# Kernel tuning notes

Hardware: AMD Instinct MI355X
Metric: run time of the kernel (lower is better)

The kernel has to match this reference:

```python
import jax, jax.numpy as jnp
import numpy as np


def _log_adjacency(feats, temperature):
    """'ours' euclidean adjacency: -pairwise_dist * exp(temperature), row log_softmax."""
    B = feats.shape[0]
    f = feats.reshape(B, -1)                      # (B, D)
    diff = f[:, None, :] - f[None, :, :]          # (B, B, D) as in the torch code
    sq = jnp.sum(diff * diff, axis=-1)            # (B, B) squared distances
    # safe sqrt: zero distance on the diagonal, zero (sub)gradient like torch norm
    dist = jnp.where(sq > 0, jnp.sqrt(jnp.where(sq > 0, sq, 1.0)), 0.0)
    pre_softmax = -dist * jnp.exp(temperature)
    return jax.nn.log_softmax(pre_softmax, axis=1)


def setup_inputs() -> dict:
    key = jax.random.key(0)
    k1, k2 = jax.random.split(key)
    B, C, P, D = 128, 64, 32, 128
    image_feats = jax.random.normal(k1, (B, C, D), dtype=jnp.float32)
    lang_feats = jax.random.normal(k2, (B, P, D), dtype=jnp.float32)
    temperature = jnp.float32(np.log(0.5))  # learnable temperature param init
    return {"image_feats": image_feats, "lang_feats": lang_feats, "temperature": temperature}


def reference(image_feats, lang_feats, temperature):
    A_f = _log_adjacency(image_feats, temperature)   # (B, B) log-probs
    A_g = _log_adjacency(lang_feats, temperature)    # (B, B) log-probs (log target)
    # F.kl_div(A_f, A_g, log_target=True, reduction='none') = exp(A_g) * (A_g - A_f)
    kl = jnp.exp(A_g) * (A_g - A_f)
    return kl.sum(axis=0)                            # (B,)
```

## Files before the change

### kernel.cpp

```cpp
#include <hip/hip_runtime.h>
#include <hip/hip_bf16.h>
#include <math.h>


#define NROW 128
#define PAIRS 16384
#define D0 8192
#define D1 4096
#define CK 64
#define NC0 128
#define NC1 64
#define NCHUNK 192

typedef short v8s  __attribute__((ext_vector_type(8)));
typedef float v16f __attribute__((ext_vector_type(16)));

union Frag {
    v8s s;
    __hip_bfloat162 h[4];
};

__device__ __forceinline__ void splitPair(float a, float b, Frag& hi, Frag& lo, int idx) {
    __hip_bfloat162 h = __float22bfloat162_rn(make_float2(a, b));
    const float ra = a - __bfloat162float(h.x);
    const float rb = b - __bfloat162float(h.y);
    __hip_bfloat162 l = __float22bfloat162_rn(make_float2(ra, rb));
    hi.h[idx] = h;
    lo.h[idx] = l;
}

__device__ __forceinline__ void loadFrag(const float* __restrict__ p, Frag& hi, Frag& lo) {
    const float4 v0 = *(const float4*)(p);
    const float4 v1 = *(const float4*)(p + 4);
    splitPair(v0.x, v0.y, hi, lo, 0);
    splitPair(v0.z, v0.w, hi, lo, 1);
    splitPair(v1.x, v1.y, hi, lo, 2);
    splitPair(v1.z, v1.w, hi, lo, 3);
}

__global__ __launch_bounds__(256) void k_gram(
    const float* __restrict__ F0, const float* __restrict__ F1,
    float* __restrict__ partials, float* __restrict__ diagP,
    float* __restrict__ out)
{
    const int b = blockIdx.x;
    const int t = threadIdx.x;
    if (b == 0 && t < NROW) out[t] = 0.0f;

    const float* F; int D, k0;
    if (b < NC0) { F = F0; D = D0; k0 = b * CK; }
    else         { F = F1; D = D1; k0 = (b - NC0) * CK; }

    const int wave  = t >> 6;
    const int wy    = wave >> 1;
    const int wx    = wave & 1;
    const int lane  = t & 63;
    const int r32   = lane & 31;
    const int khalf = lane >> 5;

    const int rA0 = wy * 64 + r32;
    const int rA1 = wy * 64 + 32 + r32;
    const int rB0 = wx * 64 + r32;
    const int rB1 = wx * 64 + 32 + r32;

    v16f acc[2][2];
#pragma unroll
    for (int ti = 0; ti < 2; ++ti)
#pragma unroll
        for (int tj = 0; tj < 2; ++tj)
#pragma unroll
            for (int r = 0; r < 16; ++r) acc[ti][tj][r] = 0.0f;

#pragma unroll
    for (int g = 0; g < CK / 16; ++g) {
        const int col = k0 + g * 16 + khalf * 8;
        Frag Ah[2], Al[2], Bh[2], Bl[2];
        loadFrag(F + (size_t)rA0 * D + col, Ah[0], Al[0]);
        loadFrag(F + (size_t)rA1 * D + col, Ah[1], Al[1]);
        loadFrag(F + (size_t)rB0 * D + col, Bh[0], Bl[0]);
        loadFrag(F + (size_t)rB1 * D + col, Bh[1], Bl[1]);
#pragma unroll
        for (int ti = 0; ti < 2; ++ti)
#pragma unroll
            for (int tj = 0; tj < 2; ++tj) {
                acc[ti][tj] = __builtin_amdgcn_mfma_f32_32x32x16_bf16(
                    Ah[ti].s, Bh[tj].s, acc[ti][tj], 0, 0, 0);
                acc[ti][tj] = __builtin_amdgcn_mfma_f32_32x32x16_bf16(
                    Ah[ti].s, Bl[tj].s, acc[ti][tj], 0, 0, 0);
                acc[ti][tj] = __builtin_amdgcn_mfma_f32_32x32x16_bf16(
                    Al[ti].s, Bh[tj].s, acc[ti][tj], 0, 0, 0);
                acc[ti][tj] = __builtin_amdgcn_mfma_f32_32x32x16_bf16(
                    Al[ti].s, Bl[tj].s, acc[ti][tj], 0, 0, 0);
            }
    }

    float* __restrict__ pout = partials + (size_t)b * PAIRS;
#pragma unroll
    for (int ti = 0; ti < 2; ++ti)
#pragma unroll
        for (int tj = 0; tj < 2; ++tj) {
            const int rowbase = wy * 64 + ti * 32;
            const int n = wx * 64 + tj * 32 + r32;
#pragma unroll
            for (int r = 0; r < 16; ++r) {
                const int m = rowbase + (r & 3) + 8 * (r >> 2) + 4 * khalf;
                const float v = acc[ti][tj][r];
                pout[m * NROW + n] = v;
                if (m == n) diagP[b * NROW + m] = v;
            }
        }
}

__device__ __forceinline__ float waveMax64(float v) {
#pragma unroll
    for (int off = 32; off > 0; off >>= 1) v = fmaxf(v, __shfl_xor(v, off, 64));
    return v;
}
__device__ __forceinline__ float waveSum64(float v) {
#pragma unroll
    for (int off = 32; off > 0; off >>= 1) v += __shfl_xor(v, off, 64);
    return v;
}

__global__ __launch_bounds__(256) void k_kl(
    const float* __restrict__ partials, const float* __restrict__ diagP,
    const float* __restrict__ temp, float* __restrict__ out)
{
    __shared__ float red[4];
    __shared__ float gii_s[2];
    __shared__ float Arow[2][NROW];

    const int i = blockIdx.x;
    const int t = threadIdx.x;
    const int s = t >> 7;
    const int j = t & 127;
    const int w = t >> 6;
    const float et = expf(temp[0]);

    const int   base = s ? NC0 : 0;
    const int   nc   = s ? NC1 : NC0;
    const float* Ps  = partials + (size_t)base * PAIRS;
    const float* Ds  = diagP + base * NROW;

    float a0 = 0.f, a1 = 0.f, a2 = 0.f, a3 = 0.f;
    {
        const float* p = Ps + i * NROW + j;
        for (int c = 0; c < nc; c += 4) {
            a0 += p[(size_t)(c + 0) * PAIRS];
            a1 += p[(size_t)(c + 1) * PAIRS];
            a2 += p[(size_t)(c + 2) * PAIRS];
            a3 += p[(size_t)(c + 3) * PAIRS];
        }
    }
    const float gij = (a0 + a1) + (a2 + a3);

    float d0 = 0.f, d1 = 0.f, d2 = 0.f, d3 = 0.f;
    {
        const float* p = Ds + j;
        for (int c = 0; c < nc; c += 4) {
            d0 += p[(c + 0) * NROW];
            d1 += p[(c + 1) * NROW];
            d2 += p[(c + 2) * NROW];
            d3 += p[(c + 3) * NROW];
        }
    }
    const float gjj = (d0 + d1) + (d2 + d3);

    if (j == i) gii_s[s] = gjj;
    __syncthreads();
    const float gii = gii_s[s];

    const float sq   = (i == j) ? 0.0f : (gii + gjj - 2.0f * gij);
    const float dist = sq > 0.0f ? sqrtf(sq) : 0.0f;
    const float pre  = -dist * et;

    float m = waveMax64(pre);
    if ((t & 63) == 0) red[w] = m;
    __syncthreads();
    m = fmaxf(red[2 * s], red[2 * s + 1]);
    __syncthreads();

    float e = expf(pre - m);
    float sum = waveSum64(e);
    if ((t & 63) == 0) red[w] = sum;
    __syncthreads();
    sum = red[2 * s] + red[2 * s + 1];

    const float A = pre - (m + logf(sum));
    Arow[s][j] = A;
    __syncthreads();

    if (s == 0) {
        const float Af = Arow[0][j];
        const float Ag = Arow[1][j];
        atomicAdd(out + j, expf(Ag) * (Ag - Af));
    }
}

extern "C" void kernel_launch(void* const* d_in, const int* in_sizes, int n_in,
                              void* d_out, int out_size, void* d_ws, size_t ws_size,
                              hipStream_t stream)
{
    const float* img  = (const float*)d_in[0];
    const float* lng  = (const float*)d_in[1];
    const float* temp = (const float*)d_in[2];
    float* out = (float*)d_out;

    float* partials = (float*)d_ws;
    float* diagP    = partials + (size_t)NCHUNK * PAIRS;

    k_gram<<<NCHUNK, 256, 0, stream>>>(img, lng, partials, diagP, out);
    k_kl<<<NROW, 256, 0, stream>>>(partials, diagP, temp, out);
}
```

Measured before the change: 87.90 us.

## Fuse gram and KL kernels into one cooperative launch with grid sync

Merges the partial-Gram MFMA kernel and the log-softmax/KL reduction kernel into one cooperative kernel separated by a grid-wide barrier. This removes the second launch and the gap between the two kernels. The partial-sum loop is also widened from 4 to 8 accumulators to put more loads in flight. The cost is the overhead of cooperative launch and grid sync, plus the constraint that all 192 blocks must be co-resident.

```diff
diff --git a/kernel.cpp b/kernel.cpp
--- a/kernel.cpp
+++ b/kernel.cpp
@@ -1,6 +1,9 @@
 #include <hip/hip_runtime.h>
 #include <hip/hip_bf16.h>
+#include <hip/hip_cooperative_groups.h>
 #include <math.h>
+
+namespace cg = cooperative_groups;
 
 
 #define NROW 128
@@ -38,162 +41,162 @@
     splitPair(v1.z, v1.w, hi, lo, 3);
 }
 
-__global__ __launch_bounds__(256) void k_gram(
+__device__ __forceinline__ float waveMax64(float v) {
+#pragma unroll
+    for (int off = 32; off > 0; off >>= 1) v = fmaxf(v, __shfl_xor(v, off, 64));
+    return v;
+}
+__device__ __forceinline__ float waveSum64(float v) {
+#pragma unroll
+    for (int off = 32; off > 0; off >>= 1) v += __shfl_xor(v, off, 64);
+    return v;
+}
+
+__global__ __launch_bounds__(256) void k_fused(
     const float* __restrict__ F0, const float* __restrict__ F1,
     float* __restrict__ partials, float* __restrict__ diagP,
-    float* __restrict__ out)
+    const float* __restrict__ temp, float* __restrict__ out)
 {
     const int b = blockIdx.x;
     const int t = threadIdx.x;
     if (b == 0 && t < NROW) out[t] = 0.0f;
 
-    const float* F; int D, k0;
-    if (b < NC0) { F = F0; D = D0; k0 = b * CK; }
-    else         { F = F1; D = D1; k0 = (b - NC0) * CK; }
-
-    const int wave  = t >> 6;
-    const int wy    = wave >> 1;
-    const int wx    = wave & 1;
-    const int lane  = t & 63;
-    const int r32   = lane & 31;
-    const int khalf = lane >> 5;
-
-    const int rA0 = wy * 64 + r32;
-    const int rA1 = wy * 64 + 32 + r32;
-    const int rB0 = wx * 64 + r32;
-    const int rB1 = wx * 64 + 32 + r32;
-
-    v16f acc[2][2];
-#pragma unroll
-    for (int ti = 0; ti < 2; ++ti)
-#pragma unroll
-        for (int tj = 0; tj < 2; ++tj)
-#pragma unroll
-            for (int r = 0; r < 16; ++r) acc[ti][tj][r] = 0.0f;
-
-#pragma unroll
-    for (int g = 0; g < CK / 16; ++g) {
-        const int col = k0 + g * 16 + khalf * 8;
-        Frag Ah[2], Al[2], Bh[2], Bl[2];
-        loadFrag(F + (size_t)rA0 * D + col, Ah[0], Al[0]);
-        loadFrag(F + (size_t)rA1 * D + col, Ah[1], Al[1]);
-        loadFrag(F + (size_t)rB0 * D + col, Bh[0], Bl[0]);
-        loadFrag(F + (size_t)rB1 * D + col, Bh[1], Bl[1]);
+    {
+        const float* F; int D, k0;
+        if (b < NC0) { F = F0; D = D0; k0 = b * CK; }
+        else         { F = F1; D = D1; k0 = (b - NC0) * CK; }
+
+        const int wave  = t >> 6;
+        const int wy    = wave >> 1;
+        const int wx    = wave & 1;
+        const int lane  = t & 63;
+        const int r32   = lane & 31;
+        const int khalf = lane >> 5;
+
+        const int rA0 = wy * 64 + r32;
+        const int rA1 = wy * 64 + 32 + r32;
+        const int rB0 = wx * 64 + r32;
+        const int rB1 = wx * 64 + 32 + r32;
+
+        v16f acc[2][2];
 #pragma unroll
         for (int ti = 0; ti < 2; ++ti)
 #pragma unroll
+            for (int tj = 0; tj < 2; ++tj)
+#pragma unroll
+                for (int r = 0; r < 16; ++r) acc[ti][tj][r] = 0.0f;
+
+#pragma unroll
+        for (int g = 0; g < CK / 16; ++g) {
+            const int col = k0 + g * 16 + khalf * 8;
+            Frag Ah[2], Al[2], Bh[2], Bl[2];
+            loadFrag(F + (size_t)rA0 * D + col, Ah[0], Al[0]);
+            loadFrag(F + (size_t)rA1 * D + col, Ah[1], Al[1]);
+            loadFrag(F + (size_t)rB0 * D + col, Bh[0], Bl[0]);
+            loadFrag(F + (size_t)rB1 * D + col, Bh[1], Bl[1]);
+#pragma unroll
+            for (int ti = 0; ti < 2; ++ti)
+#pragma unroll
+                for (int tj = 0; tj < 2; ++tj) {
+                    acc[ti][tj] = __builtin_amdgcn_mfma_f32_32x32x16_bf16(
+                        Ah[ti].s, Bh[tj].s, acc[ti][tj], 0, 0, 0);
+                    acc[ti][tj] = __builtin_amdgcn_mfma_f32_32x32x16_bf16(
+                        Ah[ti].s, Bl[tj].s, acc[ti][tj], 0, 0, 0);
+                    acc[ti][tj] = __builtin_amdgcn_mfma_f32_32x32x16_bf16(
+                        Al[ti].s, Bh[tj].s, acc[ti][tj], 0, 0, 0);
+                    acc[ti][tj] = __builtin_amdgcn_mfma_f32_32x32x16_bf16(
+                        Al[ti].s, Bl[tj].s, acc[ti][tj], 0, 0, 0);
+                }
+        }
+
+        float* __restrict__ pout = partials + (size_t)b * PAIRS;
+#pragma unroll
+        for (int ti = 0; ti < 2; ++ti)
+#pragma unroll
             for (int tj = 0; tj < 2; ++tj) {
-                acc[ti][tj] = __builtin_amdgcn_mfma_f32_32x32x16_bf16(
-                    Ah[ti].s, Bh[tj].s, acc[ti][tj], 0, 0, 0);
-                acc[ti][tj] = __builtin_amdgcn_mfma_f32_32x32x16_bf16(
-                    Ah[ti].s, Bl[tj].s, acc[ti][tj], 0, 0, 0);
-                acc[ti][tj] = __builtin_amdgcn_mfma_f32_32x32x16_bf16(
-                    Al[ti].s, Bh[tj].s, acc[ti][tj], 0, 0, 0);
-                acc[ti][tj] = __builtin_amdgcn_mfma_f32_32x32x16_bf16(
-                    Al[ti].s, Bl[tj].s, acc[ti][tj], 0, 0, 0);
+                const int rowbase = wy * 64 + ti * 32;
+                const int n = wx * 64 + tj * 32 + r32;
+#pragma unroll
+                for (int r = 0; r < 16; ++r) {
+                    const int m = rowbase + (r & 3) + 8 * (r >> 2) + 4 * khalf;
+                    const float v = acc[ti][tj][r];
+                    pout[m * NROW + n] = v;
+                    if (m == n) diagP[b * NROW + m] = v;
+                }
             }
     }
 
-    float* __restrict__ pout = partials + (size_t)b * PAIRS;
-#pragma unroll
-    for (int ti = 0; ti < 2; ++ti)
-#pragma unroll
-        for (int tj = 0; tj < 2; ++tj) {
-            const int rowbase = wy * 64 + ti * 32;
-            const int n = wx * 64 + tj * 32 + r32;
-#pragma unroll
-            for (int r = 0; r < 16; ++r) {
-                const int m = rowbase + (r & 3) + 8 * (r >> 2) + 4 * khalf;
-                const float v = acc[ti][tj][r];
-                pout[m * NROW + n] = v;
-                if (m == n) diagP[b * NROW + m] = v;
+    cg::this_grid().sync();
+
+    if (b < NROW) {
+        __shared__ float red[4];
+        __shared__ float gii_s[2];
+        __shared__ float Arow[2][NROW];
+
+        const int i = b;
+        const int s = t >> 7;
+        const int j = t & 127;
+        const int w = t >> 6;
+        const float et = expf(temp[0]);
+
+        const int   base = s ? NC0 : 0;
+        const int   nc   = s ? NC1 : NC0;
+        const float* Ps  = partials + (size_t)base * PAIRS;
+        const float* Ds  = diagP + base * NROW;
+
+        float a[8];
+#pragma unroll
+        for (int u = 0; u < 8; ++u) a[u] = 0.0f;
+        {
+            const float* p = Ps + i * NROW + j;
+            for (int c = 0; c < nc; c += 8) {
+#pragma unroll
+                for (int u = 0; u < 8; ++u) a[u] += p[(size_t)(c + u) * PAIRS];
             }
         }
-}
-
-__device__ __forceinline__ float waveMax64(float v) {
-#pragma unroll
-    for (int off = 32; off > 0; off >>= 1) v = fmaxf(v, __shfl_xor(v, off, 64));
-    return v;
-}
-__device__ __forceinline__ float waveSum64(float v) {
-#pragma unroll
-    for (int off = 32; off > 0; off >>= 1) v += __shfl_xor(v, off, 64);
-    return v;
-}
-
-__global__ __launch_bounds__(256) void k_kl(
-    const float* __restrict__ partials, const float* __restrict__ diagP,
-    const float* __restrict__ temp, float* __restrict__ out)
-{
-    __shared__ float red[4];
-    __shared__ float gii_s[2];
-    __shared__ float Arow[2][NROW];
-
-    const int i = blockIdx.x;
-    const int t = threadIdx.x;
-    const int s = t >> 7;
-    const int j = t & 127;
-    const int w = t >> 6;
-    const float et = expf(temp[0]);
-
-    const int   base = s ? NC0 : 0;
-    const int   nc   = s ? NC1 : NC0;
-    const float* Ps  = partials + (size_t)base * PAIRS;
-    const float* Ds  = diagP + base * NROW;
-
-    float a0 = 0.f, a1 = 0.f, a2 = 0.f, a3 = 0.f;
-    {
-        const float* p = Ps + i * NROW + j;
-        for (int c = 0; c < nc; c += 4) {
-            a0 += p[(size_t)(c + 0) * PAIRS];
-            a1 += p[(size_t)(c + 1) * PAIRS];
-            a2 += p[(size_t)(c + 2) * PAIRS];
-            a3 += p[(size_t)(c + 3) * PAIRS];
-        }
-    }
-    const float gij = (a0 + a1) + (a2 + a3);
-
-    float d0 = 0.f, d1 = 0.f, d2 = 0.f, d3 = 0.f;
-    {
-        const float* p = Ds + j;
-        for (int c = 0; c < nc; c += 4) {
-            d0 += p[(c + 0) * NROW];
-            d1 += p[(c + 1) * NROW];
-            d2 += p[(c + 2) * NROW];
-            d3 += p[(c + 3) * NROW];
-        }
-    }
-    const float gjj = (d0 + d1) + (d2 + d3);
-
-    if (j == i) gii_s[s] = gjj;
-    __syncthreads();
-    const float gii = gii_s[s];
-
-    const float sq   = (i == j) ? 0.0f : (gii + gjj - 2.0f * gij);
-    const float dist = sq > 0.0f ? sqrtf(sq) : 0.0f;
-    const float pre  = -dist * et;
-
-    float m = waveMax64(pre);
-    if ((t & 63) == 0) red[w] = m;
-    __syncthreads();
-    m = fmaxf(red[2 * s], red[2 * s + 1]);
-    __syncthreads();
-
-    float e = expf(pre - m);
-    float sum = waveSum64(e);
-    if ((t & 63) == 0) red[w] = sum;
-    __syncthreads();
-    sum = red[2 * s] + red[2 * s + 1];
-
-    const float A = pre - (m + logf(sum));
-    Arow[s][j] = A;
-    __syncthreads();
-
-    if (s == 0) {
-        const float Af = Arow[0][j];
-        const float Ag = Arow[1][j];
-        atomicAdd(out + j, expf(Ag) * (Ag - Af));
+        const float gij = ((a[0] + a[1]) + (a[2] + a[3])) + ((a[4] + a[5]) + (a[6] + a[7]));
+
+        float d[4];
+#pragma unroll
+        for (int u = 0; u < 4; ++u) d[u] = 0.0f;
+        {
+            const float* p = Ds + j;
+            for (int c = 0; c < nc; c += 4) {
+#pragma unroll
+                for (int u = 0; u < 4; ++u) d[u] += p[(c + u) * NROW];
+            }
+        }
+        const float gjj = (d[0] + d[1]) + (d[2] + d[3]);
+
+        if (j == i) gii_s[s] = gjj;
+        __syncthreads();
+        const float gii = gii_s[s];
+
+        const float sq   = (i == j) ? 0.0f : (gii + gjj - 2.0f * gij);
+        const float dist = sq > 0.0f ? sqrtf(sq) : 0.0f;
+        const float pre  = -dist * et;
+
+        float m = waveMax64(pre);
+        if ((t & 63) == 0) red[w] = m;
+        __syncthreads();
+        m = fmaxf(red[2 * s], red[2 * s + 1]);
+        __syncthreads();
+
+        float e = expf(pre - m);
+        float sum = waveSum64(e);
+        if ((t & 63) == 0) red[w] = sum;
+        __syncthreads();
+        sum = red[2 * s] + red[2 * s + 1];
+
+        const float A = pre - (m + logf(sum));
+        Arow[s][j] = A;
+        __syncthreads();
+
+        if (s == 0) {
+            const float Af = Arow[0][j];
+            const float Ag = Arow[1][j];
+            atomicAdd(out + j, expf(Ag) * (Ag - Af));
+        }
     }
 }
 
@@ -209,6 +212,8 @@
     float* partials = (float*)d_ws;
     float* diagP    = partials + (size_t)NCHUNK * PAIRS;
 
-    k_gram<<<NCHUNK, 256, 0, stream>>>(img, lng, partials, diagP, out);
-    k_kl<<<NROW, 256, 0, stream>>>(partials, diagP, temp, out);
-}
+    void* args[] = { (void*)&img, (void*)&lng, (void*)&partials,
+                     (void*)&diagP, (void*)&temp, (void*)&out };
+    hipLaunchCooperativeKernel((const void*)k_fused, dim3(NCHUNK), dim3(256),
+                               args, 0, stream);
+}
```

Measured after the change: 125.2 us. +42.4%, slower.
